# Performance work log

Hardware: AMD Instinct MI355X
Metric: run time of the kernel (lower is better)

## Reference

```python
import jax, jax.numpy as jnp
import numpy as np

D_IN = 1024
D_OUT = 1024
SEQ = 4096


def setup_inputs() -> dict:
    key = jax.random.key(0)
    k0, k1, k2, k3 = jax.random.split(key, 4)
    inputs = jax.random.normal(k0, (SEQ, D_IN), dtype=jnp.float32)
    # original uses torch.rand (uniform [0,1)) for weights
    W_q = jax.random.uniform(k1, (D_IN, D_OUT), dtype=jnp.float32)
    W_k = jax.random.uniform(k2, (D_IN, D_OUT), dtype=jnp.float32)
    W_v = jax.random.uniform(k3, (D_IN, D_OUT), dtype=jnp.float32)
    return {"inputs": inputs, "W_q": W_q, "W_k": W_k, "W_v": W_v}


def reference(inputs, W_q, W_k, W_v):
    queries = inputs @ W_q            # [S, d_out]
    keys = inputs @ W_k               # [S, d_out]
    values = inputs @ W_v             # [S, d_out]
    d_k = keys.shape[-1]
    scale = 1.0 / jnp.sqrt(jnp.asarray(d_k, dtype=queries.dtype))
    attn_scores = queries @ keys.T    # [S, S]
    attn_weights = jax.nn.softmax(attn_scores * scale, axis=-1)
    context_vectors = attn_weights @ values  # [S, d_out]
    return context_vectors
```

## Files before the change

kernel.cpp:

```cpp
#include <hip/hip_runtime.h>

typedef unsigned short u16;
typedef __attribute__((ext_vector_type(8))) short bf16x8;
typedef __attribute__((ext_vector_type(4))) float f32x4;

#define SEQ 4096
#define DIM 1024

__device__ __forceinline__ u16 f2bf(float f) {
  unsigned u = __float_as_uint(f);
  return (u16)((u + 0x7fffu + ((u >> 16) & 1u)) >> 16);
}
__device__ __forceinline__ float bf2f(u16 h) {
  return __uint_as_float(((unsigned)h) << 16);
}

__device__ __forceinline__ void gload_lds16(const void* g, void* l) {
  __builtin_amdgcn_global_load_lds(
      (const __attribute__((address_space(1))) void*)g,
      (__attribute__((address_space(3))) void*)l, 16, 0, 0);
}

#define VM0 asm volatile("s_waitcnt vmcnt(0)" ::: "memory")
#define VM4 asm volatile("s_waitcnt vmcnt(4)" ::: "memory")
#define VM8 asm volatile("s_waitcnt vmcnt(8)" ::: "memory")
#define BAR __builtin_amdgcn_s_barrier()

__device__ __forceinline__ size_t pkoff(int row, int col, int kd) {
  int tile = (row >> 7) * (kd >> 5) + (col >> 5);
  int r7 = row & 127, c5 = col & 31;
  int slot = ((r7 >> 4) << 6) | ((c5 >> 3) << 4) | (r7 & 15);
  return (size_t)tile * 4096 + (size_t)(slot * 8 + (c5 & 7));
}

__device__ __forceinline__ void stage_tile_pk(const u16* __restrict__ g,
                                              u16* lds, int tid) {
  const int w = tid >> 6;
  gload_lds16(g + (size_t)tid * 8, lds + (size_t)(w * 64) * 8);
  gload_lds16(g + (size_t)(256 + tid) * 8, lds + (size_t)(256 + w * 64) * 8);
}

__device__ __forceinline__ void stage_q512(const u16* __restrict__ g,
                                           int kb, int nkb, u16* ldsq, int tid) {
  const int w = tid >> 6;
  gload_lds16(g + (size_t)kb * 4096 + tid * 8, ldsq + w * 512);
  gload_lds16(g + ((size_t)nkb + kb) * 4096 + tid * 8, ldsq + 4096 + w * 512);
}

__device__ __forceinline__ void gemm3_256(
    const u16* __restrict__ A0, const u16* __restrict__ A1,
    const u16* __restrict__ B0, const u16* __restrict__ B1,
    int nkb, u16* lds, f32x4 (&acc)[8][4]) {
  const int tid = threadIdx.x;
  const int w = tid >> 6, l = tid & 63;
  const int wm = w >> 2, wn = w & 3;

#pragma unroll
  for (int mi = 0; mi < 8; ++mi)
#pragma unroll
    for (int ni = 0; ni < 4; ++ni)
      acc[mi][ni] = (f32x4){0.f, 0.f, 0.f, 0.f};

  const int QA0 = 0, QA1 = 8192, QB0 = 16384, QB1 = 24576;
  const int aoff = wm * 4096 + l * 8;
  const int boff = ((wn & 2) >> 1) * 4096 + (wn & 1) * 2048 + l * 8;

  stage_q512(A0, 0, nkb, lds + QA0, tid);
  stage_q512(B0, 0, nkb, lds + QB0, tid);
  stage_q512(B1, 0, nkb, lds + QB1, tid);
  stage_q512(A1, 0, nkb, lds + QA1, tid);

  for (int kb = 0; kb < nkb; ++kb) {
    u16* cur = lds + (kb & 1) * 32768;
    u16* nxt = lds + ((kb + 1) & 1) * 32768;
    const bool pf = (kb + 1 < nkb);
    bf16x8 a0[8], b0[4];

    VM4;
    BAR;
    if (pf) {
      stage_q512(A0, kb + 1, nkb, nxt + QA0, tid);
      stage_q512(B0, kb + 1, nkb, nxt + QB0, tid);
    }
#pragma unroll
    for (int i = 0; i < 8; ++i) a0[i] = *(const bf16x8*)(cur + QA0 + aoff + i * 512);
#pragma unroll
    for (int i = 0; i < 4; ++i) b0[i] = *(const bf16x8*)(cur + QB0 + boff + i * 512);
    __builtin_amdgcn_s_setprio(1);
#pragma unroll
    for (int mi = 0; mi < 8; ++mi)
#pragma unroll
      for (int ni = 0; ni < 4; ++ni)
        acc[mi][ni] = __builtin_amdgcn_mfma_f32_16x16x32_bf16(
            a0[mi], b0[ni], acc[mi][ni], 0, 0, 0);
    __builtin_amdgcn_s_setprio(0);

    if (pf) { VM4; } else { VM0; }
    BAR;
    if (pf) {
      stage_q512(B1, kb + 1, nkb, nxt + QB1, tid);
      stage_q512(A1, kb + 1, nkb, nxt + QA1, tid);
    }
    {
      bf16x8 b1[4];
#pragma unroll
      for (int i = 0; i < 4; ++i) b1[i] = *(const bf16x8*)(cur + QB1 + boff + i * 512);
      __builtin_amdgcn_s_setprio(1);
#pragma unroll
      for (int mi = 0; mi < 8; ++mi)
#pragma unroll
        for (int ni = 0; ni < 4; ++ni)
          acc[mi][ni] = __builtin_amdgcn_mfma_f32_16x16x32_bf16(
              a0[mi], b1[ni], acc[mi][ni], 0, 0, 0);
      __builtin_amdgcn_s_setprio(0);
    }
    {
      bf16x8 a1[8];
#pragma unroll
      for (int i = 0; i < 8; ++i) a1[i] = *(const bf16x8*)(cur + QA1 + aoff + i * 512);
      __builtin_amdgcn_s_setprio(1);
#pragma unroll
      for (int mi = 0; mi < 8; ++mi)
#pragma unroll
        for (int ni = 0; ni < 4; ++ni)
          acc[mi][ni] = __builtin_amdgcn_mfma_f32_16x16x32_bf16(
              a1[mi], b0[ni], acc[mi][ni], 0, 0, 0);
      __builtin_amdgcn_s_setprio(0);
    }
  }
  __syncthreads();
}

__device__ __forceinline__ void gemm1_256(
    const u16* __restrict__ A, const u16* __restrict__ B,
    int nkb, u16* lds, f32x4 (&acc)[8][4]) {
  const int tid = threadIdx.x;
  const int w = tid >> 6, l = tid & 63;
  const int wm = w >> 2, wn = w & 3;

#pragma unroll
  for (int mi = 0; mi < 8; ++mi)
#pragma unroll
    for (int ni = 0; ni < 4; ++ni)
      acc[mi][ni] = (f32x4){0.f, 0.f, 0.f, 0.f};

  const int aoff = wm * 4096 + l * 8;
  const int boff = ((wn & 2) >> 1) * 4096 + (wn & 1) * 2048 + l * 8;

  stage_q512(A, 0, nkb, lds + 0 * 16384, tid);
  stage_q512(B, 0, nkb, lds + 0 * 16384 + 8192, tid);
  stage_q512(A, 1, nkb, lds + 1 * 16384, tid);
  stage_q512(B, 1, nkb, lds + 1 * 16384 + 8192, tid);
  stage_q512(A, 2, nkb, lds + 2 * 16384, tid);
  stage_q512(B, 2, nkb, lds + 2 * 16384 + 8192, tid);

  for (int kb = 0; kb < nkb; ++kb) {
    if (kb + 2 < nkb) { VM8; } else if (kb + 1 < nkb) { VM4; } else { VM0; }
    BAR;
    if (kb + 3 < nkb) {
      u16* nb = lds + ((kb + 3) & 3) * 16384;
      stage_q512(A, kb + 3, nkb, nb, tid);
      stage_q512(B, kb + 3, nkb, nb + 8192, tid);
    }
    const u16* cb = lds + (kb & 3) * 16384;
    bf16x8 av[8], bv[4];
#pragma unroll
    for (int i = 0; i < 8; ++i) av[i] = *(const bf16x8*)(cb + aoff + i * 512);
#pragma unroll
    for (int i = 0; i < 4; ++i) bv[i] = *(const bf16x8*)(cb + 8192 + boff + i * 512);
    __builtin_amdgcn_s_setprio(1);
#pragma unroll
    for (int mi = 0; mi < 8; ++mi)
#pragma unroll
      for (int ni = 0; ni < 4; ++ni)
        acc[mi][ni] = __builtin_amdgcn_mfma_f32_16x16x32_bf16(
            av[mi], bv[ni], acc[mi][ni], 0, 0, 0);
    __builtin_amdgcn_s_setprio(0);
  }
  __syncthreads();
}

__device__ __forceinline__ void gemm1_db(
    const u16* A, const u16* B, int nkb, u16* lds, f32x4 (&acc)[4][4]) {
  const int tid = threadIdx.x;
  const int w = tid >> 6, l = tid & 63;
  const int wm = w >> 1, wn = w & 1;

#pragma unroll
  for (int mi = 0; mi < 4; ++mi)
#pragma unroll
    for (int ni = 0; ni < 4; ++ni)
      acc[mi][ni] = (f32x4){0.f, 0.f, 0.f, 0.f};

  const int ao = wm * 2048 + l * 8;
  const int bo = wn * 2048 + l * 8;
  const int nit = nkb >> 1;

  stage_tile_pk(A, lds, tid);
  stage_tile_pk(A + 4096, lds + 4096, tid);
  stage_tile_pk(B, lds + 8192, tid);
  stage_tile_pk(B + 4096, lds + 12288, tid);

  for (int it = 0; it < nit; ++it) {
    __syncthreads();
    if (it + 1 < nit) {
      u16* nb = lds + ((it + 1) & 1) * 16384;
      const size_t off = (size_t)(it + 1) * 8192;
      stage_tile_pk(A + off, nb, tid);
      stage_tile_pk(A + off + 4096, nb + 4096, tid);
      stage_tile_pk(B + off, nb + 8192, tid);
      stage_tile_pk(B + off + 4096, nb + 12288, tid);
    }
    const u16* cb = lds + (it & 1) * 16384;
#pragma unroll
    for (int ht = 0; ht < 2; ++ht) {
      bf16x8 av[4], bv[4];
#pragma unroll
      for (int i = 0; i < 4; ++i) {
        av[i] = *(const bf16x8*)(cb + ht * 4096 + ao + i * 512);
        bv[i] = *(const bf16x8*)(cb + 8192 + ht * 4096 + bo + i * 512);
      }
#pragma unroll
      for (int mi = 0; mi < 4; ++mi)
#pragma unroll
        for (int ni = 0; ni < 4; ++ni)
          acc[mi][ni] = __builtin_amdgcn_mfma_f32_16x16x32_bf16(
              av[mi], bv[ni], acc[mi][ni], 0, 0, 0);
    }
  }
  __syncthreads();
}

#define EPILOGUE_IDX                                          \
  const int tid = threadIdx.x, w = tid >> 6, l = tid & 63;    \
  const int wm = w >> 1, wn = w & 1, lr = l & 15, q = l >> 4; \
  (void)tid;

__device__ __forceinline__ void epilogue_pack256(
    f32x4 (&acc)[8][4], u16* lds, int row0, int col0, int kd,
    u16* __restrict__ H, u16* __restrict__ L) {
  const int tid = threadIdx.x, w = tid >> 6, l = tid & 63;
  const int wm = w >> 2, wn = w & 3, lr = l & 15, q = l >> 4;
  float* lC = (float*)lds;
#pragma unroll
  for (int p = 0; p < 4; ++p) {
    if (wm == (p >> 1)) {
      const int mib = (p & 1) * 4;
#pragma unroll
      for (int mi2 = 0; mi2 < 4; ++mi2)
#pragma unroll
        for (int ni = 0; ni < 4; ++ni)
#pragma unroll
          for (int r = 0; r < 4; ++r)
            lC[(mi2 * 16 + q * 4 + r) * 260 + wn * 64 + ni * 16 + lr] =
                acc[mib + mi2][ni][r];
    }
    __syncthreads();
#pragma unroll
    for (int j = 0; j < 2; ++j) {
      int u = tid + 512 * j;
      int row = u >> 4, c0 = (u & 15) * 16;
      u16 hbuf[16], lbuf[16];
#pragma unroll
      for (int i = 0; i < 16; ++i) {
        float v = lC[row * 260 + c0 + i];
        u16 hv = f2bf(v);
        hbuf[i] = hv;
        lbuf[i] = f2bf(v - bf2f(hv));
      }
      int rg = row0 + p * 64 + row;
      size_t o0 = pkoff(rg, col0 + c0, kd);
      size_t o1 = pkoff(rg, col0 + c0 + 8, kd);
      *(bf16x8*)(H + o0) = *(bf16x8*)(hbuf);
      *(bf16x8*)(H + o1) = *(bf16x8*)(hbuf + 8);
      if (L) {
        *(bf16x8*)(L + o0) = *(bf16x8*)(lbuf);
        *(bf16x8*)(L + o1) = *(bf16x8*)(lbuf + 8);
      }
    }
    if (p < 3) __syncthreads();
  }
}


__global__ __launch_bounds__(256) void prep_kernel(
    const float* __restrict__ X,
    const float* __restrict__ W0, const float* __restrict__ W1, const float* __restrict__ W2,
    u16* __restrict__ Xh, u16* __restrict__ Xl,
    u16* __restrict__ H0, u16* __restrict__ L0,
    u16* __restrict__ H1, u16* __restrict__ L1,
    u16* __restrict__ H2) {
  const int z = blockIdx.z;
  const int tx = threadIdx.x, ty = threadIdx.y;
  if (z == 0) {
    int idx = (blockIdx.y * 32 + blockIdx.x) * 256 + ty * 32 + tx;
    int row = idx >> 6;
    int c0 = (idx & 63) * 16;
    u16 h[16], lo[16];
#pragma unroll
    for (int j = 0; j < 4; ++j) {
      float4 x = *(const float4*)(X + (size_t)row * DIM + c0 + j * 4);
      float v;
      v = x.x; h[j*4+0] = f2bf(v); lo[j*4+0] = f2bf(v - bf2f(h[j*4+0]));
      v = x.y; h[j*4+1] = f2bf(v); lo[j*4+1] = f2bf(v - bf2f(h[j*4+1]));
      v = x.z; h[j*4+2] = f2bf(v); lo[j*4+2] = f2bf(v - bf2f(h[j*4+2]));
      v = x.w; h[j*4+3] = f2bf(v); lo[j*4+3] = f2bf(v - bf2f(h[j*4+3]));
    }
    size_t o0 = pkoff(row, c0, DIM);
    size_t o1 = pkoff(row, c0 + 8, DIM);
    *(bf16x8*)(Xh + o0) = *(bf16x8*)(h);
    *(bf16x8*)(Xl + o0) = *(bf16x8*)(lo);
    *(bf16x8*)(Xh + o1) = *(bf16x8*)(h + 8);
    *(bf16x8*)(Xl + o1) = *(bf16x8*)(lo + 8);
    return;
  }
  __shared__ float t[32][33];
  const float* W = (z == 1) ? W0 : (z == 2) ? W1 : W2;
  u16* H = (z == 1) ? H0 : (z == 2) ? H1 : H2;
  u16* L = (z == 1) ? L0 : (z == 2) ? L1 : nullptr;
  const int i0 = blockIdx.y * 32, o0 = blockIdx.x * 32;
#pragma unroll
  for (int m = 0; m < 4; ++m)
    t[ty + 8 * m][tx] = W[(size_t)(i0 + ty + 8 * m) * DIM + o0 + tx];
  __syncthreads();
#pragma unroll
  for (int m = 0; m < 4; ++m) {
    float v = t[tx][ty + 8 * m];
    u16 h = f2bf(v);
    size_t o = pkoff(o0 + ty + 8 * m, i0 + tx, DIM);
    H[o] = h;
    if (L) L[o] = f2bf(v - bf2f(h));
  }
}

__global__ __launch_bounds__(512, 2) void qkv_kernel(
    const u16* __restrict__ Xh, const u16* __restrict__ Xl,
    const u16* __restrict__ Wh0, const u16* __restrict__ Wl0,
    const u16* __restrict__ Wh1, const u16* __restrict__ Wl1,
    const u16* __restrict__ Wh2,
    u16* __restrict__ Qh, u16* __restrict__ Ql,
    u16* __restrict__ Kh, u16* __restrict__ Kl,
    u16* __restrict__ VT) {
  __shared__ __align__(16) u16 lds[2 * 32768];
  const int z = blockIdx.z;
  const int bid = blockIdx.y * 4 + blockIdx.x;
  const int xcd = bid & 7, c = bid >> 3;
  const int Y = xcd * 2 + (c >> 2);
  const int Xp = c & 3;
  f32x4 acc[8][4];
  if (z < 2) {
    const u16* Wh = z ? Wh1 : Wh0;
    const u16* Wl = z ? Wl1 : Wl0;
    const int row0 = Y * 256;
    const int col0 = Xp * 256;
    gemm3_256(Xh + (size_t)row0 * DIM, Xl + (size_t)row0 * DIM,
              Wh + (size_t)col0 * DIM, Wl + (size_t)col0 * DIM,
              DIM / 32, lds, acc);
    epilogue_pack256(acc, lds, row0, col0, DIM, z ? Kh : Qh, z ? Kl : Ql);
  } else {
    const int row0 = Xp * 256;
    const int col0 = Y * 256;
    gemm1_256(Wh2 + (size_t)row0 * DIM, Xh + (size_t)col0 * DIM,
              DIM / 32, lds, acc);
    epilogue_pack256(acc, lds, row0, col0, SEQ, VT, nullptr);
  }
}

__global__ __launch_bounds__(512, 2) void s_kernel(
    const u16* __restrict__ Qh, const u16* __restrict__ Ql,
    const u16* __restrict__ Kh, const u16* __restrict__ Kl,
    float* __restrict__ S) {
  __shared__ __align__(16) u16 lds[2 * 32768];
  const int bid = blockIdx.y * 16 + blockIdx.x;
  const int xcd = bid & 7, c = bid >> 3;
  const int Y = (xcd & 3) * 4 + (c >> 3);
  const int X = (xcd >> 2) * 8 + (c & 7);
  const int row0 = Y * 256, col0 = X * 256;
  f32x4 acc[8][4];
  gemm3_256(Qh + (size_t)row0 * DIM, Ql + (size_t)row0 * DIM,
            Kh + (size_t)col0 * DIM, Kl + (size_t)col0 * DIM,
            DIM / 32, lds, acc);
  const int tid = threadIdx.x, w = tid >> 6, l = tid & 63;
  const int wm = w >> 2, wn = w & 3, lr = l & 15, q = l >> 4;
  const float scale = 0.03125f;
#pragma unroll
  for (int mi = 0; mi < 8; ++mi)
#pragma unroll
    for (int ni = 0; ni < 4; ++ni)
#pragma unroll
      for (int r = 0; r < 4; ++r) {
        int row = row0 + wm * 128 + mi * 16 + q * 4 + r;
        int col = col0 + wn * 64 + ni * 16 + lr;
        S[(size_t)row * SEQ + col] = acc[mi][ni][r] * scale;
      }
}

__global__ __launch_bounds__(256) void softmax_kernel(const float* __restrict__ S,
                                                      u16* __restrict__ P) {
  const int row = blockIdx.x;
  const float* s = S + (size_t)row * SEQ;
  const int tid = threadIdx.x;
  const int c0 = tid * 16;
  float v[16];
  float mx = -3.4e38f;
#pragma unroll
  for (int j = 0; j < 4; ++j) {
    float4 x = *(const float4*)(s + c0 + j * 4);
    v[j * 4 + 0] = x.x; v[j * 4 + 1] = x.y; v[j * 4 + 2] = x.z; v[j * 4 + 3] = x.w;
    mx = fmaxf(mx, fmaxf(fmaxf(x.x, x.y), fmaxf(x.z, x.w)));
  }
#pragma unroll
  for (int off = 32; off; off >>= 1) mx = fmaxf(mx, __shfl_xor(mx, off));
  __shared__ float red[8];
  const int w = tid >> 6, l = tid & 63;
  if (l == 0) red[w] = mx;
  __syncthreads();
  mx = fmaxf(fmaxf(red[0], red[1]), fmaxf(red[2], red[3]));
  float sum = 0.f;
#pragma unroll
  for (int i = 0; i < 16; ++i) {
    v[i] = __expf(v[i] - mx);
    sum += v[i];
  }
#pragma unroll
  for (int off = 32; off; off >>= 1) sum += __shfl_xor(sum, off);
  if (l == 0) red[4 + w] = sum;
  __syncthreads();
  sum = red[4] + red[5] + red[6] + red[7];
  const float inv = 1.f / sum;
  u16 p[16];
#pragma unroll
  for (int i = 0; i < 16; ++i) p[i] = f2bf(v[i] * inv);
  *(bf16x8*)(P + pkoff(row, c0, SEQ)) = *(bf16x8*)(p);
  *(bf16x8*)(P + pkoff(row, c0 + 8, SEQ)) = *(bf16x8*)(p + 8);
}

__global__ __launch_bounds__(256) void o_kernel(const u16* __restrict__ P,
                                                const u16* __restrict__ VT,
                                                float* __restrict__ O) {
  __shared__ __align__(16) u16 lds[2 * 4 * 4096];
  const int bid = blockIdx.y * 8 + blockIdx.x;
  const int xcd = bid & 7, c = bid >> 3;
  const int Y = xcd * 4 + (c >> 3);
  const int X = c & 7;
  const int row0 = Y * 128, col0 = X * 128;
  const u16* A = P + (size_t)row0 * SEQ;
  const u16* B = VT + (size_t)col0 * SEQ;
  f32x4 acc[4][4];
  gemm1_db(A, B, 128, lds, acc);
  EPILOGUE_IDX
#pragma unroll
  for (int mi = 0; mi < 4; ++mi)
#pragma unroll
    for (int ni = 0; ni < 4; ++ni)
#pragma unroll
      for (int r = 0; r < 4; ++r) {
        int row = row0 + wm * 64 + mi * 16 + q * 4 + r;
        int col = col0 + wn * 64 + ni * 16 + lr;
        O[(size_t)row * DIM + col] = acc[mi][ni][r];
      }
}

extern "C" void kernel_launch(void* const* d_in, const int* in_sizes, int n_in,
                              void* d_out, int out_size, void* d_ws, size_t ws_size,
                              hipStream_t stream) {
  const float* X = (const float*)d_in[0];
  const float* Wq = (const float*)d_in[1];
  const float* Wk = (const float*)d_in[2];
  const float* Wv = (const float*)d_in[3];

  const size_t MB = 1024 * 1024;
  char* w = (char*)d_ws;
  u16* Xh = (u16*)(w + 0 * MB);
  u16* Xl = (u16*)(w + 8 * MB);
  u16* WqhT = (u16*)(w + 16 * MB);
  u16* WqlT = (u16*)(w + 18 * MB);
  u16* WkhT = (u16*)(w + 20 * MB);
  u16* WklT = (u16*)(w + 22 * MB);
  u16* WvhT = (u16*)(w + 24 * MB);
  u16* Qh = (u16*)(w + 26 * MB);
  u16* Ql = (u16*)(w + 34 * MB);
  u16* Kh = (u16*)(w + 42 * MB);
  u16* Kl = (u16*)(w + 50 * MB);
  u16* VT = (u16*)(w + 58 * MB);
  float* S = (float*)(w + 66 * MB);
  u16* P = (u16*)(w + 26 * MB);

  prep_kernel<<<dim3(32, 32, 4), dim3(32, 8), 0, stream>>>(
      X, Wq, Wk, Wv, Xh, Xl, WqhT, WqlT, WkhT, WklT, WvhT);
  qkv_kernel<<<dim3(DIM / 256, SEQ / 256, 3), 512, 0, stream>>>(
      Xh, Xl, WqhT, WqlT, WkhT, WklT, WvhT, Qh, Ql, Kh, Kl, VT);
  s_kernel<<<dim3(SEQ / 256, SEQ / 256), 512, 0, stream>>>(Qh, Ql, Kh, Kl, S);
  softmax_kernel<<<SEQ, 256, 0, stream>>>(S, P);
  o_kernel<<<dim3(DIM / 128, SEQ / 128), 256, 0, stream>>>(P, VT, (float*)d_out);
}
```

Baseline: 307.9 us.

## Replace double-buffered PV GEMM loop with 4-stage async pipeline

The P·V output GEMM previously staged two k-blocks per iteration into a double buffer with a full barrier each iteration. It now uses a 4-slot ring buffer with three k-blocks in flight, and waits only on the specific outstanding global-to-LDS loads via vmcnt counts before each barrier. MFMA sections are raised with s_setprio, and launch bounds now request two blocks per CU. This is meant to hide global load latency better and reduce barrier stalls. The trade-off is more reliance on correct vmcnt accounting and possible register pressure from the occupancy hint.

```diff
diff --git a/kernel.cpp b/kernel.cpp
--- a/kernel.cpp
+++ b/kernel.cpp
@@ -180,8 +180,9 @@
   __syncthreads();
 }
 
-__device__ __forceinline__ void gemm1_db(
-    const u16* A, const u16* B, int nkb, u16* lds, f32x4 (&acc)[4][4]) {
+__device__ __forceinline__ void gemm1_ctd128(
+    const u16* __restrict__ A, const u16* __restrict__ B,
+    int nkb, u16* lds, f32x4 (&acc)[4][4]) {
   const int tid = threadIdx.x;
   const int w = tid >> 6, l = tid & 63;
   const int wm = w >> 1, wn = w & 1;
@@ -194,39 +195,38 @@
 
   const int ao = wm * 2048 + l * 8;
   const int bo = wn * 2048 + l * 8;
-  const int nit = nkb >> 1;
-
-  stage_tile_pk(A, lds, tid);
-  stage_tile_pk(A + 4096, lds + 4096, tid);
-  stage_tile_pk(B, lds + 8192, tid);
-  stage_tile_pk(B + 4096, lds + 12288, tid);
-
-  for (int it = 0; it < nit; ++it) {
-    __syncthreads();
-    if (it + 1 < nit) {
-      u16* nb = lds + ((it + 1) & 1) * 16384;
-      const size_t off = (size_t)(it + 1) * 8192;
+
+  stage_tile_pk(A, lds + 0 * 8192, tid);
+  stage_tile_pk(B, lds + 0 * 8192 + 4096, tid);
+  stage_tile_pk(A + 4096, lds + 1 * 8192, tid);
+  stage_tile_pk(B + 4096, lds + 1 * 8192 + 4096, tid);
+  stage_tile_pk(A + 8192, lds + 2 * 8192, tid);
+  stage_tile_pk(B + 8192, lds + 2 * 8192 + 4096, tid);
+
+  for (int kb = 0; kb < nkb; ++kb) {
+    if (kb + 2 < nkb) { VM8; } else if (kb + 1 < nkb) { VM4; } else { VM0; }
+    BAR;
+    if (kb + 3 < nkb) {
+      u16* nb = lds + ((kb + 3) & 3) * 8192;
+      const size_t off = (size_t)(kb + 3) * 4096;
       stage_tile_pk(A + off, nb, tid);
-      stage_tile_pk(A + off + 4096, nb + 4096, tid);
-      stage_tile_pk(B + off, nb + 8192, tid);
-      stage_tile_pk(B + off + 4096, nb + 12288, tid);
-    }
-    const u16* cb = lds + (it & 1) * 16384;
-#pragma unroll
-    for (int ht = 0; ht < 2; ++ht) {
-      bf16x8 av[4], bv[4];
-#pragma unroll
-      for (int i = 0; i < 4; ++i) {
-        av[i] = *(const bf16x8*)(cb + ht * 4096 + ao + i * 512);
-        bv[i] = *(const bf16x8*)(cb + 8192 + ht * 4096 + bo + i * 512);
-      }
-#pragma unroll
-      for (int mi = 0; mi < 4; ++mi)
-#pragma unroll
-        for (int ni = 0; ni < 4; ++ni)
-          acc[mi][ni] = __builtin_amdgcn_mfma_f32_16x16x32_bf16(
-              av[mi], bv[ni], acc[mi][ni], 0, 0, 0);
-    }
+      stage_tile_pk(B + off, nb + 4096, tid);
+    }
+    const u16* cb = lds + (kb & 3) * 8192;
+    bf16x8 av[4], bv[4];
+#pragma unroll
+    for (int i = 0; i < 4; ++i) {
+      av[i] = *(const bf16x8*)(cb + ao + i * 512);
+      bv[i] = *(const bf16x8*)(cb + 4096 + bo + i * 512);
+    }
+    __builtin_amdgcn_s_setprio(1);
+#pragma unroll
+    for (int mi = 0; mi < 4; ++mi)
+#pragma unroll
+      for (int ni = 0; ni < 4; ++ni)
+        acc[mi][ni] = __builtin_amdgcn_mfma_f32_16x16x32_bf16(
+            av[mi], bv[ni], acc[mi][ni], 0, 0, 0);
+    __builtin_amdgcn_s_setprio(0);
   }
   __syncthreads();
 }
@@ -435,10 +435,10 @@
   *(bf16x8*)(P + pkoff(row, c0 + 8, SEQ)) = *(bf16x8*)(p + 8);
 }
 
-__global__ __launch_bounds__(256) void o_kernel(const u16* __restrict__ P,
-                                                const u16* __restrict__ VT,
-                                                float* __restrict__ O) {
-  __shared__ __align__(16) u16 lds[2 * 4 * 4096];
+__global__ __launch_bounds__(256, 2) void o_kernel(const u16* __restrict__ P,
+                                                   const u16* __restrict__ VT,
+                                                   float* __restrict__ O) {
+  __shared__ __align__(16) u16 lds[4 * 8192];
   const int bid = blockIdx.y * 8 + blockIdx.x;
   const int xcd = bid & 7, c = bid >> 3;
   const int Y = xcd * 4 + (c >> 3);
@@ -447,7 +447,7 @@
   const u16* A = P + (size_t)row0 * SEQ;
   const u16* B = VT + (size_t)col0 * SEQ;
   f32x4 acc[4][4];
-  gemm1_db(A, B, 128, lds, acc);
+  gemm1_ctd128(A, B, 128, lds, acc);
   EPILOGUE_IDX
 #pragma unroll
   for (int mi = 0; mi < 4; ++mi)
```

After: 307.9 us. No clear change (-0.0%).
